# Performance work log

Measured on AMD Instinct MI355X. Metric: run time of the kernel, lower is better.

The kernel has to match this reference:

```python
import math
import jax, jax.numpy as jnp
import numpy as np

D_MODEL = 1024
NUM_HEAD = 16
HEAD_DIM = 64
B = 4
S = 1024


def setup_inputs() -> dict:
    key = jax.random.key(0)
    ks = jax.random.split(key, 11)
    scale = 1.0 / math.sqrt(D_MODEL)
    inp = {
        "x": jax.random.normal(ks[0], (B, S, D_MODEL), dtype=jnp.float32),
        "y": jax.random.normal(ks[1], (B, S, D_MODEL), dtype=jnp.float32),
        "mask": jnp.zeros((S, S), dtype=jnp.float32),
        "Wq": jax.random.uniform(ks[2], (D_MODEL, D_MODEL), jnp.float32, -scale, scale),
        "bq": jax.random.uniform(ks[3], (D_MODEL,), jnp.float32, -scale, scale),
        "Wk": jax.random.uniform(ks[4], (D_MODEL, D_MODEL), jnp.float32, -scale, scale),
        "bk": jax.random.uniform(ks[5], (D_MODEL,), jnp.float32, -scale, scale),
        "Wv": jax.random.uniform(ks[6], (D_MODEL, D_MODEL), jnp.float32, -scale, scale),
        "bv": jax.random.uniform(ks[7], (D_MODEL,), jnp.float32, -scale, scale),
        "Wo": jax.random.uniform(ks[8], (D_MODEL, D_MODEL), jnp.float32, -scale, scale),
        "bo": jax.random.uniform(ks[9], (D_MODEL,), jnp.float32, -scale, scale),
    }
    return inp


def _split_heads(t):
    # (B, S, D) -> (B, H, S, hd)
    b, s, _ = t.shape
    return t.reshape(b, s, NUM_HEAD, HEAD_DIM).transpose(0, 2, 1, 3)


def reference(x, y, mask, Wq, bq, Wk, bk, Wv, bv, Wo, bo):
    q = _split_heads(y @ Wq.T + bq)  # (B, H, S, hd)
    k = _split_heads(x @ Wk.T + bk)
    v = _split_heads(x @ Wv.T + bv)
    scaled = jnp.einsum("bhqd,bhkd->bhqk", q, k) / math.sqrt(HEAD_DIM)
    # torch: scaled.permute(1,0,2,3) + mask  -> (H, B, S, S); second permute is a no-op
    scaled = scaled.transpose(1, 0, 2, 3) + mask
    attention = jax.nn.softmax(scaled, axis=-1)
    attention = jnp.where(jnp.isnan(attention), 0.0, attention)
    # torch sum(dim=1) on (H, B, S, S) sums over BATCH -> (H, S, S)
    attention = jnp.sum(attention, axis=1)
    # broadcast matmul: (H, S, S) @ (B, H, S, hd) -> (B, H, S, hd)
    V = jnp.einsum("hqk,bhkd->bhqd", attention, v)
    V = V.transpose(0, 2, 1, 3).reshape(B, S, NUM_HEAD * HEAD_DIM)
    return V @ Wo.T + bo
```

## Files before the change

kernel.cpp:

```cpp
#include <hip/hip_runtime.h>

typedef unsigned short u16;
typedef unsigned int   u32;
typedef __attribute__((ext_vector_type(8))) short short8;
typedef __attribute__((ext_vector_type(4))) float floatx4;

#define DEV static __device__ __forceinline__

constexpr int S_  = 1024;
constexpr int Dm  = 1024;
constexpr int HD  = 64;


DEV u16 f2b(float f) {
  u32 u = __builtin_bit_cast(u32, f);
  u = u + 0x7fffu + ((u >> 16) & 1u);
  return (u16)(u >> 16);
}
DEV float b2f(u16 h) { u32 u = ((u32)h) << 16; return __builtin_bit_cast(float, u); }

DEV void gld16(const u16* g, u16* l) {
  __builtin_amdgcn_global_load_lds(
      (const __attribute__((address_space(1))) u32*)g,
      (__attribute__((address_space(3))) u32*)l, 16, 0, 0);
}

template<int ROWS, int NT>
DEV void stage_tile(const u16* src, long stride, long kOff, u16* lds, int tid) {
  constexpr int NBLK = ROWS * 8;
  constexpr int NISS = NBLK / NT;
  static_assert(NBLK % NT == 0, "");
  int w = tid >> 6;
  #pragma unroll
  for (int i = 0; i < NISS; ++i) {
    int bi = i * NT + tid;
    int m  = bi >> 3;
    int kb = (bi & 7) ^ (m & 7);
    const u16* g = src + (long)m * stride + kOff + (kb << 3);
    u16* l = lds + ((long)(i * NT + (w << 6)) << 3);
    gld16(g, l);
  }
}

DEV short8 read_frag(const u16* lds, int m, int kb) {
  int off = (m << 6) + ((kb ^ (m & 7)) << 3);
  return *(const short8*)(lds + off);
}

DEV floatx4 mfma16(short8 a, short8 b, floatx4 c) {
  return __builtin_amdgcn_mfma_f32_16x16x32_bf16(a, b, c, 0, 0, 0);
}


struct CvtArgs { const float* s[6]; u16* d[6]; };

__global__ __launch_bounds__(256)
void cvt_all(CvtArgs a) {
  int b = blockIdx.x;
  int t, lb;
  if (b < 4096)      { t = 0; lb = b; }
  else if (b < 8192) { t = 1; lb = b - 4096; }
  else               { t = 2 + ((b - 8192) >> 10); lb = (b - 8192) & 1023; }
  int i = (lb * 256 + (int)threadIdx.x) * 4;
  float4 v = *(const float4*)(a.s[t] + i);
  u32 lo = (u32)f2b(v.x) | ((u32)f2b(v.y) << 16);
  u32 hi = (u32)f2b(v.z) | ((u32)f2b(v.w) << 16);
  uint2 o; o.x = lo; o.y = hi;
  *(uint2*)(a.d[t] + i) = o;
}


__global__ __launch_bounds__(256)
void emask_prep(const float* __restrict__ mask, u16* __restrict__ em,
                u16* __restrict__ emr) {
  __shared__ u16 lp[8 * 1024];
  int tid = threadIdx.x;
  long q0 = (long)blockIdx.x * 8;
  #pragma unroll
  for (int rr = 0; rr < 8; ++rr) {
    long q = q0 + rr;
    float4 v = *(const float4*)(mask + q * 1024 + tid * 4);
    u16 e0 = f2b(__expf(v.x)), e1 = f2b(__expf(v.y));
    u16 e2 = f2b(__expf(v.z)), e3 = f2b(__expf(v.w));
    u32 lo = (u32)e0 | ((u32)e1 << 16);
    u32 hi = (u32)e2 | ((u32)e3 << 16);
    uint2 o; o.x = lo; o.y = hi;
    *(uint2*)(em + q * 1024 + tid * 4) = o;
    int k = tid * 4;
    u16 es[4] = {e0, e1, e2, e3};
    #pragma unroll
    for (int j = 0; j < 4; ++j) {
      int kk = k + j;
      lp[rr * 1024 + ((kk & 15) << 6) + (kk >> 4)] = es[j];
    }
  }
  __syncthreads();
  #pragma unroll
  for (int jj = 0; jj < 4; ++jj) {
    int o = jj * 2048 + tid * 8;
    uint4 v = *(const uint4*)(lp + o);
    *(uint4*)(emr + q0 * 1024 + o) = v;
  }
}


struct QkvArgs { const u16* A[3]; const u16* W[3]; const float* bias[3]; u16* C[3]; };

__global__ __launch_bounds__(256, 2)
void gemm_qkv(QkvArgs args) {
  constexpr int CPAD = 136;
  __shared__ u16 smem[128 * CPAD];
  u16* lA = smem;
  u16* lB = smem + 8192;
  int tid = threadIdx.x, lane = tid & 63, w = tid >> 6;
  int wm = w & 1, wn = w >> 1;
  int sel = blockIdx.z;
  bool vt = (sel == 2);
  float scl = (sel == 0) ? 0.125f : 1.0f;
  long mBase = (long)blockIdx.y * 128;
  long nBase = (long)blockIdx.x * 128;
  const u16* Ab = args.A[sel] + mBase * (long)Dm;
  const u16* Bb = args.W[sel] + nBase * (long)Dm;
  const float* bias = args.bias[sel];
  u16* C = args.C[sel];

  floatx4 acc[4][4];
  #pragma unroll
  for (int i = 0; i < 4; ++i)
    #pragma unroll
    for (int j = 0; j < 4; ++j) acc[i][j] = floatx4{0.f, 0.f, 0.f, 0.f};

  for (int kt = 0; kt < Dm; kt += 64) {
    __syncthreads();
    stage_tile<128, 256>(Ab, Dm, kt, lA, tid);
    stage_tile<128, 256>(Bb, Dm, kt, lB, tid);
    __syncthreads();
    #pragma unroll
    for (int ks = 0; ks < 2; ++ks) {
      short8 af[4], bf[4];
      #pragma unroll
      for (int mi = 0; mi < 4; ++mi)
        af[mi] = read_frag(lA, wm*64 + mi*16 + (lane & 15), ks*4 + (lane >> 4));
      #pragma unroll
      for (int ni = 0; ni < 4; ++ni)
        bf[ni] = read_frag(lB, wn*64 + ni*16 + (lane & 15), ks*4 + (lane >> 4));
      #pragma unroll
      for (int mi = 0; mi < 4; ++mi)
        #pragma unroll
        for (int ni = 0; ni < 4; ++ni)
          acc[mi][ni] = mfma16(af[mi], bf[ni], acc[mi][ni]);
    }
  }

  __syncthreads();
  #pragma unroll
  for (int mi = 0; mi < 4; ++mi) {
    int rowb = wm*64 + mi*16 + ((lane >> 4) << 2);
    #pragma unroll
    for (int ni = 0; ni < 4; ++ni) {
      int col = wn*64 + ni*16 + (lane & 15);
      float bv = bias[nBase + col];
      #pragma unroll
      for (int r = 0; r < 4; ++r) {
        float v = (acc[mi][ni][r] + bv) * scl;
        if (!vt) smem[(rowb + r) * CPAD + col] = f2b(v);
        else     smem[col * CPAD + (rowb + r)] = f2b(v);
      }
    }
  }
  __syncthreads();
  #pragma unroll
  for (int i = 0; i < 8; ++i) {
    int idx = (i * 256 + tid) * 8;
    int r0 = idx >> 7, c0 = idx & 127;
    uint4 v = *(const uint4*)(smem + r0 * CPAD + c0);
    if (!vt) {
      *(uint4*)(C + (mBase + r0) * (long)Dm + nBase + c0) = v;
    } else {
      long m = mBase + c0;
      long ad = ((m >> 10) << 20) + ((nBase + r0) << 10) + (m & 1023);
      *(uint4*)(C + ad) = v;
    }
  }
}


constexpr int MO_BF16 = 0, MO_F32 = 1;

template<int BM, int BN, int WM, int WN, int MODE, bool BIAS, bool ZBH>
__global__ __launch_bounds__(WM*WN*64, 2)
void gemm_bt(const u16* __restrict__ A, const u16* __restrict__ Bmat,
             const float* __restrict__ bias, void* __restrict__ C,
             int K, int ldc) {
  constexpr int NT   = WM * WN * 64;
  constexpr int MI   = BM / WM / 16;
  constexpr int NI   = BN / WN / 16;
  constexpr int WROW = BM / WM;
  constexpr int WCOL = BN / WN;
  constexpr int STG  = (BM + BN) * 64;
  constexpr int CPAD = BN + 8;
  constexpr int CSZ  = BM * CPAD;
  constexpr int SM   = (MODE == MO_F32) ? STG : (STG > CSZ ? STG : CSZ);
  __shared__ u16 smem[SM];
  u16* lA = smem;
  u16* lB = smem + BM * 64;

  int tid = threadIdx.x, lane = tid & 63, w = tid >> 6;
  int wm = w % WM, wn = w / WM;
  long mBase = (long)blockIdx.y * BM;
  long nBase = (long)blockIdx.x * BN;
  long aOff = 0, bOff = 0, cOff = 0;
  if (ZBH) {
    int z = blockIdx.z, bz = z >> 4, h = z & 15;
    aOff = (long)h << 20;
    bOff = (long)z << 16;
    cOff = ((long)bz << 20) + h * HD;
  }
  const u16* Ab = A + aOff + mBase * (long)K;
  const u16* Bb = Bmat + bOff + nBase * (long)K;

  floatx4 acc[MI][NI];
  #pragma unroll
  for (int i = 0; i < MI; ++i)
    #pragma unroll
    for (int j = 0; j < NI; ++j) acc[i][j] = floatx4{0.f, 0.f, 0.f, 0.f};

  for (int kt = 0; kt < K; kt += 64) {
    __syncthreads();
    stage_tile<BM, NT>(Ab, K, kt, lA, tid);
    stage_tile<BN, NT>(Bb, K, kt, lB, tid);
    __syncthreads();
    #pragma unroll
    for (int ks = 0; ks < 2; ++ks) {
      short8 af[MI], bf[NI];
      #pragma unroll
      for (int mi = 0; mi < MI; ++mi)
        af[mi] = read_frag(lA, wm*WROW + mi*16 + (lane & 15), ks*4 + (lane >> 4));
      #pragma unroll
      for (int ni = 0; ni < NI; ++ni)
        bf[ni] = read_frag(lB, wn*WCOL + ni*16 + (lane & 15), ks*4 + (lane >> 4));
      #pragma unroll
      for (int mi = 0; mi < MI; ++mi)
        #pragma unroll
        for (int ni = 0; ni < NI; ++ni)
          acc[mi][ni] = mfma16(af[mi], bf[ni], acc[mi][ni]);
    }
  }

  if (MODE == MO_F32) {
    #pragma unroll
    for (int mi = 0; mi < MI; ++mi) {
      int rowb = wm*WROW + mi*16 + ((lane >> 4) << 2);
      #pragma unroll
      for (int ni = 0; ni < NI; ++ni) {
        int col = wn*WCOL + ni*16 + (lane & 15);
        long n = nBase + col;
        float bv = BIAS ? bias[n] : 0.f;
        #pragma unroll
        for (int r = 0; r < 4; ++r)
          ((float*)C)[cOff + (mBase + rowb + r) * (long)ldc + n] = acc[mi][ni][r] + bv;
      }
    }
  } else {
    __syncthreads();
    #pragma unroll
    for (int mi = 0; mi < MI; ++mi) {
      int rowb = wm*WROW + mi*16 + ((lane >> 4) << 2);
      #pragma unroll
      for (int ni = 0; ni < NI; ++ni) {
        int col = wn*WCOL + ni*16 + (lane & 15);
        float bv = BIAS ? bias[nBase + col] : 0.f;
        #pragma unroll
        for (int r = 0; r < 4; ++r)
          smem[(rowb + r) * CPAD + col] = f2b(acc[mi][ni][r] + bv);
      }
    }
    __syncthreads();
    constexpr int TOT = BM * BN;
    #pragma unroll
    for (int i = 0; i < TOT / (NT * 8); ++i) {
      int idx = (i * NT + tid) * 8;
      int r0 = idx / BN, c0 = idx % BN;
      uint4 v = *(const uint4*)(smem + r0 * CPAD + c0);
      *(uint4*)((u16*)C + cOff + (mBase + r0) * (long)ldc + nBase + c0) = v;
    }
  }
}


__global__ __launch_bounds__(256)
void attn_stats(const u16* __restrict__ Q, const u16* __restrict__ Kw,
                const u16* __restrict__ emr, float* __restrict__ lPart) {
  __shared__ u16 lQ[128 * 64];
  __shared__ u16 lK[2][128 * 64];
  int tid = threadIdx.x, lane = tid & 63, w = tid >> 6;
  int qT = blockIdx.x, h = blockIdx.y, z = blockIdx.z;
  int b = z >> 1, c = z & 1;
  const u16* Qb = Q + ((long)b << 20) + h * HD + (long)qT * 128 * Dm;
  const u16* Kb = Kw + ((long)b << 20) + h * HD + (long)c * 512 * Dm;

  stage_tile<128, 256>(Qb, Dm, 0, lQ, tid);
  stage_tile<128, 256>(Kb, Dm, 0, lK[0], tid);
  __syncthreads();

  short8 af[2][2];
  #pragma unroll
  for (int mi = 0; mi < 2; ++mi)
    #pragma unroll
    for (int ks = 0; ks < 2; ++ks)
      af[mi][ks] = read_frag(lQ, w*32 + mi*16 + (lane & 15), ks*4 + (lane >> 4));

  float lsum[2][4];
  #pragma unroll
  for (int mi = 0; mi < 2; ++mi)
    #pragma unroll
    for (int r = 0; r < 4; ++r) lsum[mi][r] = 0.f;

  for (int kt = 0; kt < 4; ++kt) {
    if (kt < 3)
      stage_tile<128, 256>(Kb + (long)(kt + 1) * 128 * Dm, Dm, 0, lK[(kt + 1) & 1], tid);
    const u16* lKc = lK[kt & 1];
    floatx4 sc[2][8];
    #pragma unroll
    for (int mi = 0; mi < 2; ++mi)
      #pragma unroll
      for (int ni = 0; ni < 8; ++ni) sc[mi][ni] = floatx4{0.f, 0.f, 0.f, 0.f};
    #pragma unroll
    for (int ks = 0; ks < 2; ++ks) {
      short8 bf[8];
      #pragma unroll
      for (int ni = 0; ni < 8; ++ni)
        bf[ni] = read_frag(lKc, ni*16 + (lane & 15), ks*4 + (lane >> 4));
      #pragma unroll
      for (int mi = 0; mi < 2; ++mi)
        #pragma unroll
        for (int ni = 0; ni < 8; ++ni)
          sc[mi][ni] = mfma16(af[mi][ks], bf[ni], sc[mi][ni]);
    }
    int q0w = qT*128 + w*32;
    int iBase = (c*512 + kt*128) >> 4;
    #pragma unroll
    for (int mi = 0; mi < 2; ++mi)
      #pragma unroll
      for (int r = 0; r < 4; ++r) {
        int q = q0w + mi*16 + ((lane >> 4) << 2) + r;
        uint4 ev = *(const uint4*)(emr + ((long)q << 10) + ((lane & 15) << 6) + iBase);
        const u16* e8 = (const u16*)&ev;
        float a = 0.f;
        #pragma unroll
        for (int ni = 0; ni < 8; ++ni)
          a += __expf(sc[mi][ni][r]) * b2f(e8[ni]);
        lsum[mi][r] += a;
      }
    if (kt < 3) __syncthreads();
  }
  #pragma unroll
  for (int mi = 0; mi < 2; ++mi)
    #pragma unroll
    for (int r = 0; r < 4; ++r) {
      float l = lsum[mi][r];
      #pragma unroll
      for (int off = 1; off < 16; off <<= 1) l += __shfl_xor(l, off);
      if ((lane & 15) == 0) {
        int q = qT*128 + w*32 + mi*16 + ((lane >> 4) << 2) + r;
        lPart[(long)c * 65536 + ((long)(b * 16 + h) << 10) + q] = l;
      }
    }
}


__global__ __launch_bounds__(256)
void attn_probs(const u16* __restrict__ Q, const u16* __restrict__ Kw,
                const u16* __restrict__ em, const float* __restrict__ lPart,
                u16* __restrict__ att) {
  constexpr int CPAD = 136;
  __shared__ u16 smem[4 * 8192];
  __shared__ float lL[512];
  int tid = threadIdx.x, lane = tid & 63, w = tid >> 6;
  int wm = w & 1, wn = w >> 1;
  int kT = blockIdx.x, qT = blockIdx.y, h = blockIdx.z;
  long q0 = (long)qT * 128, k0 = (long)kT * 128;

  stage_tile<128, 256>(Q + h * HD + q0 * Dm, Dm, 0, smem, tid);
  stage_tile<128, 256>(Kw + h * HD + k0 * Dm, Dm, 0, smem + 8192, tid);
  #pragma unroll
  for (int j = 0; j < 2; ++j) {
    int t = tid + j * 256;
    int bb = t >> 7, qq = t & 127;
    long base = ((long)(bb * 16 + h) << 10) + q0 + qq;
    float l = lPart[base] + lPart[65536 + base];
    lL[t] = (l > 0.f) ? 1.f / l : 0.f;
  }
  __syncthreads();

  floatx4 pa[4][4];
  #pragma unroll
  for (int i = 0; i < 4; ++i)
    #pragma unroll
    for (int j = 0; j < 4; ++j) pa[i][j] = floatx4{0.f, 0.f, 0.f, 0.f};

  for (int b = 0; b < 4; ++b) {
    u16* buf = smem + (b & 1) * 16384;
    if (b < 3) {
      u16* nb = smem + ((b + 1) & 1) * 16384;
      stage_tile<128, 256>(Q + ((long)(b+1) << 20) + h * HD + q0 * Dm, Dm, 0, nb, tid);
      stage_tile<128, 256>(Kw + ((long)(b+1) << 20) + h * HD + k0 * Dm, Dm, 0, nb + 8192, tid);
    }
    floatx4 sc[4][4];
    #pragma unroll
    for (int i = 0; i < 4; ++i)
      #pragma unroll
      for (int j = 0; j < 4; ++j) sc[i][j] = floatx4{0.f, 0.f, 0.f, 0.f};
    #pragma unroll
    for (int ks = 0; ks < 2; ++ks) {
      short8 af[4], bf[4];
      #pragma unroll
      for (int mi = 0; mi < 4; ++mi)
        af[mi] = read_frag(buf, wm*64 + mi*16 + (lane & 15), ks*4 + (lane >> 4));
      #pragma unroll
      for (int ni = 0; ni < 4; ++ni)
        bf[ni] = read_frag(buf + 8192, wn*64 + ni*16 + (lane & 15), ks*4 + (lane >> 4));
      #pragma unroll
      for (int mi = 0; mi < 4; ++mi)
        #pragma unroll
        for (int ni = 0; ni < 4; ++ni)
          sc[mi][ni] = mfma16(af[mi], bf[ni], sc[mi][ni]);
    }
    #pragma unroll
    for (int mi = 0; mi < 4; ++mi)
      #pragma unroll
      for (int r = 0; r < 4; ++r) {
        int qq = wm*64 + mi*16 + ((lane >> 4) << 2) + r;
        float li = lL[(b << 7) + qq];
        #pragma unroll
        for (int ni = 0; ni < 4; ++ni)
          pa[mi][ni][r] += __expf(sc[mi][ni][r]) * li;
      }
    if (b < 3) __syncthreads();
  }

  __syncthreads();
  #pragma unroll
  for (int mi = 0; mi < 4; ++mi)
    #pragma unroll
    for (int ni = 0; ni < 4; ++ni) {
      int kc = wn*64 + ni*16 + (lane & 15);
      #pragma unroll
      for (int r = 0; r < 4; ++r) {
        int qq = wm*64 + mi*16 + ((lane >> 4) << 2) + r;
        smem[qq * CPAD + kc] = f2b(pa[mi][ni][r]);
      }
    }
  __syncthreads();
  #pragma unroll
  for (int i = 0; i < 8; ++i) {
    int idx = (i * 256 + tid) * 8;
    int r0 = idx >> 7, c0 = idx & 127;
    uint4 v  = *(const uint4*)(smem + r0 * CPAD + c0);
    uint4 ev = *(const uint4*)(em + (q0 + r0) * S_ + k0 + c0);
    const u16* pv = (const u16*)&v;
    const u16* ee = (const u16*)&ev;
    u16 ov[8];
    #pragma unroll
    for (int j = 0; j < 8; ++j) ov[j] = f2b(b2f(pv[j]) * b2f(ee[j]));
    *(uint4*)(att + ((long)h << 20) + (q0 + r0) * S_ + k0 + c0) = *(uint4*)ov;
  }
}


extern "C" void kernel_launch(void* const* d_in, const int* in_sizes, int n_in,
                              void* d_out, int out_size, void* d_ws, size_t ws_size,
                              hipStream_t stream) {
  const float* x    = (const float*)d_in[0];
  const float* y    = (const float*)d_in[1];
  const float* mask = (const float*)d_in[2];
  const float* Wq   = (const float*)d_in[3];
  const float* bq   = (const float*)d_in[4];
  const float* Wk   = (const float*)d_in[5];
  const float* bk   = (const float*)d_in[6];
  const float* Wv   = (const float*)d_in[7];
  const float* bv   = (const float*)d_in[8];
  const float* Wo   = (const float*)d_in[9];
  const float* bo   = (const float*)d_in[10];

  char* ws = (char*)d_ws;
  const long MB = 1024 * 1024;
  u16*  Qw   = (u16*)(ws + 0);
  u16*  Kw   = (u16*)(ws + 8 * MB);
  u16*  Vt   = (u16*)(ws + 16 * MB);
  u16*  attv = (u16*)(ws + 24 * MB);
  float* lPart = (float*)(ws + 24 * MB);
  u16*  em   = (u16*)(ws + 25 * MB);
  u16*  emr  = (u16*)(ws + 27 * MB);
  u16*  Wob  = (u16*)(ws + 33 * MB);
  u16*  att  = (u16*)(ws + 35 * MB);
  u16*  yb   = (u16*)(ws + 35 * MB);
  u16*  xb   = (u16*)(ws + 43 * MB);
  u16*  Wqb  = (u16*)(ws + 51 * MB);
  u16*  Wkb  = (u16*)(ws + 53 * MB);
  u16*  Wvb  = (u16*)(ws + 55 * MB);

  dim3 blk(256);
  CvtArgs ca;
  ca.s[0] = y;  ca.s[1] = x;  ca.s[2] = Wq;  ca.s[3] = Wk;  ca.s[4] = Wv;  ca.s[5] = Wo;
  ca.d[0] = yb; ca.d[1] = xb; ca.d[2] = Wqb; ca.d[3] = Wkb; ca.d[4] = Wvb; ca.d[5] = Wob;
  cvt_all<<<dim3(12288), blk, 0, stream>>>(ca);
  emask_prep<<<dim3(128), blk, 0, stream>>>(mask, em, emr);

  QkvArgs qa;
  qa.A[0] = yb;  qa.A[1] = xb;  qa.A[2] = xb;
  qa.W[0] = Wqb; qa.W[1] = Wkb; qa.W[2] = Wvb;
  qa.bias[0] = bq; qa.bias[1] = bk; qa.bias[2] = bv;
  qa.C[0] = Qw;  qa.C[1] = Kw;  qa.C[2] = Vt;
  gemm_qkv<<<dim3(8, 32, 3), blk, 0, stream>>>(qa);

  attn_stats<<<dim3(8, 16, 8), blk, 0, stream>>>(Qw, Kw, emr, lPart);
  attn_probs<<<dim3(8, 8, 16), blk, 0, stream>>>(Qw, Kw, em, lPart, att);

  gemm_bt<128,64,2,2,MO_BF16,false,true><<<dim3(1, 8, 64), blk, 0, stream>>>(att, Vt, nullptr, attv, 1024, 1024);
  gemm_bt<64,128,2,2,MO_F32,true,false><<<dim3(8, 64), blk, 0, stream>>>(attv, Wob, bo, d_out, 1024, 1024);
}
```

Baseline: 252.3 us.

## Load attention MFMA fragments directly from global memory, split stats over four key chunks

In attn_stats and attn_probs, Q and K fragments are now read straight from global memory into registers instead of being staged through LDS with double buffering. This removes the LDS staging work and most __syncthreads barriers. attn_stats also splits the key range into four 256-key chunks instead of two, doubling its grid, and attn_probs sums four partial row sums. The trade-off is strided 16-byte global loads, with Q and K tiles re-read by several waves through the caches. The lPart workspace must now hold twice as many partials.

```diff
diff --git a/kernel.cpp b/kernel.cpp
--- a/kernel.cpp
+++ b/kernel.cpp
@@ -45,6 +45,10 @@
 DEV short8 read_frag(const u16* lds, int m, int kb) {
   int off = (m << 6) + ((kb ^ (m & 7)) << 3);
   return *(const short8*)(lds + off);
+}
+
+DEV short8 gfrag(const u16* base, long stride, int ks, int lane) {
+  return *(const short8*)(base + (long)(lane & 15) * stride + ks * 32 + ((lane >> 4) << 3));
 }
 
 DEV floatx4 mfma16(short8 a, short8 b, floatx4 c) {
@@ -291,24 +295,18 @@
 __global__ __launch_bounds__(256)
 void attn_stats(const u16* __restrict__ Q, const u16* __restrict__ Kw,
                 const u16* __restrict__ emr, float* __restrict__ lPart) {
-  __shared__ u16 lQ[128 * 64];
-  __shared__ u16 lK[2][128 * 64];
   int tid = threadIdx.x, lane = tid & 63, w = tid >> 6;
   int qT = blockIdx.x, h = blockIdx.y, z = blockIdx.z;
-  int b = z >> 1, c = z & 1;
-  const u16* Qb = Q + ((long)b << 20) + h * HD + (long)qT * 128 * Dm;
-  const u16* Kb = Kw + ((long)b << 20) + h * HD + (long)c * 512 * Dm;
-
-  stage_tile<128, 256>(Qb, Dm, 0, lQ, tid);
-  stage_tile<128, 256>(Kb, Dm, 0, lK[0], tid);
-  __syncthreads();
+  int b = z >> 2, c = z & 3;
+  const u16* Qb = Q + ((long)b << 20) + h * HD + (long)(qT * 128 + w * 32) * Dm;
+  const u16* Kb = Kw + ((long)b << 20) + h * HD + (long)c * 256 * Dm;
 
   short8 af[2][2];
   #pragma unroll
   for (int mi = 0; mi < 2; ++mi)
     #pragma unroll
     for (int ks = 0; ks < 2; ++ks)
-      af[mi][ks] = read_frag(lQ, w*32 + mi*16 + (lane & 15), ks*4 + (lane >> 4));
+      af[mi][ks] = gfrag(Qb + (long)mi * 16 * Dm, Dm, ks, lane);
 
   float lsum[2][4];
   #pragma unroll
@@ -316,10 +314,9 @@
     #pragma unroll
     for (int r = 0; r < 4; ++r) lsum[mi][r] = 0.f;
 
-  for (int kt = 0; kt < 4; ++kt) {
-    if (kt < 3)
-      stage_tile<128, 256>(Kb + (long)(kt + 1) * 128 * Dm, Dm, 0, lK[(kt + 1) & 1], tid);
-    const u16* lKc = lK[kt & 1];
+  #pragma unroll
+  for (int kt = 0; kt < 2; ++kt) {
+    const u16* Kt = Kb + (long)kt * 128 * Dm;
     floatx4 sc[2][8];
     #pragma unroll
     for (int mi = 0; mi < 2; ++mi)
@@ -330,7 +327,7 @@
       short8 bf[8];
       #pragma unroll
       for (int ni = 0; ni < 8; ++ni)
-        bf[ni] = read_frag(lKc, ni*16 + (lane & 15), ks*4 + (lane >> 4));
+        bf[ni] = gfrag(Kt + (long)ni * 16 * Dm, Dm, ks, lane);
       #pragma unroll
       for (int mi = 0; mi < 2; ++mi)
         #pragma unroll
@@ -338,7 +335,7 @@
           sc[mi][ni] = mfma16(af[mi][ks], bf[ni], sc[mi][ni]);
     }
     int q0w = qT*128 + w*32;
-    int iBase = (c*512 + kt*128) >> 4;
+    int iBase = (c*256 + kt*128) >> 4;
     #pragma unroll
     for (int mi = 0; mi < 2; ++mi)
       #pragma unroll
@@ -352,7 +349,6 @@
           a += __expf(sc[mi][ni][r]) * b2f(e8[ni]);
         lsum[mi][r] += a;
       }
-    if (kt < 3) __syncthreads();
   }
   #pragma unroll
   for (int mi = 0; mi < 2; ++mi)
@@ -374,21 +370,19 @@
                 const u16* __restrict__ em, const float* __restrict__ lPart,
                 u16* __restrict__ att) {
   constexpr int CPAD = 136;
-  __shared__ u16 smem[4 * 8192];
+  __shared__ u16 smem[128 * CPAD];
   __shared__ float lL[512];
   int tid = threadIdx.x, lane = tid & 63, w = tid >> 6;
   int wm = w & 1, wn = w >> 1;
   int kT = blockIdx.x, qT = blockIdx.y, h = blockIdx.z;
   long q0 = (long)qT * 128, k0 = (long)kT * 128;
 
-  stage_tile<128, 256>(Q + h * HD + q0 * Dm, Dm, 0, smem, tid);
-  stage_tile<128, 256>(Kw + h * HD + k0 * Dm, Dm, 0, smem + 8192, tid);
   #pragma unroll
   for (int j = 0; j < 2; ++j) {
     int t = tid + j * 256;
     int bb = t >> 7, qq = t & 127;
     long base = ((long)(bb * 16 + h) << 10) + q0 + qq;
-    float l = lPart[base] + lPart[65536 + base];
+    float l = lPart[base] + lPart[65536 + base] + lPart[131072 + base] + lPart[196608 + base];
     lL[t] = (l > 0.f) ? 1.f / l : 0.f;
   }
   __syncthreads();
@@ -399,13 +393,10 @@
     #pragma unroll
     for (int j = 0; j < 4; ++j) pa[i][j] = floatx4{0.f, 0.f, 0.f, 0.f};
 
+  #pragma unroll
   for (int b = 0; b < 4; ++b) {
-    u16* buf = smem + (b & 1) * 16384;
-    if (b < 3) {
-      u16* nb = smem + ((b + 1) & 1) * 16384;
-      stage_tile<128, 256>(Q + ((long)(b+1) << 20) + h * HD + q0 * Dm, Dm, 0, nb, tid);
-      stage_tile<128, 256>(Kw + ((long)(b+1) << 20) + h * HD + k0 * Dm, Dm, 0, nb + 8192, tid);
-    }
+    const u16* Qb = Q + ((long)b << 20) + h * HD + (q0 + wm * 64) * Dm;
+    const u16* Kb = Kw + ((long)b << 20) + h * HD + (k0 + wn * 64) * Dm;
     floatx4 sc[4][4];
     #pragma unroll
     for (int i = 0; i < 4; ++i)
@@ -416,10 +407,10 @@
       short8 af[4], bf[4];
       #pragma unroll
       for (int mi = 0; mi < 4; ++mi)
-        af[mi] = read_frag(buf, wm*64 + mi*16 + (lane & 15), ks*4 + (lane >> 4));
+        af[mi] = gfrag(Qb + (long)mi * 16 * Dm, Dm, ks, lane);
       #pragma unroll
       for (int ni = 0; ni < 4; ++ni)
-        bf[ni] = read_frag(buf + 8192, wn*64 + ni*16 + (lane & 15), ks*4 + (lane >> 4));
+        bf[ni] = gfrag(Kb + (long)ni * 16 * Dm, Dm, ks, lane);
       #pragma unroll
       for (int mi = 0; mi < 4; ++mi)
         #pragma unroll
@@ -436,10 +427,8 @@
         for (int ni = 0; ni < 4; ++ni)
           pa[mi][ni][r] += __expf(sc[mi][ni][r]) * li;
       }
-    if (b < 3) __syncthreads();
-  }
-
-  __syncthreads();
+  }
+
   #pragma unroll
   for (int mi = 0; mi < 4; ++mi)
     #pragma unroll
@@ -514,7 +503,7 @@
   qa.C[0] = Qw;  qa.C[1] = Kw;  qa.C[2] = Vt;
   gemm_qkv<<<dim3(8, 32, 3), blk, 0, stream>>>(qa);
 
-  attn_stats<<<dim3(8, 16, 8), blk, 0, stream>>>(Qw, Kw, emr, lPart);
+  attn_stats<<<dim3(8, 16, 16), blk, 0, stream>>>(Qw, Kw, emr, lPart);
   attn_probs<<<dim3(8, 8, 16), blk, 0, stream>>>(Qw, Kw, em, lPart, att);
 
   gemm_bt<128,64,2,2,MO_BF16,false,true><<<dim3(1, 8, 64), blk, 0, stream>>>(att, Vt, nullptr, attv, 1024, 1024);
```

New measurement: 286.4 us. 13.5% more time.
